# Kernel tuning notes

Measured on AMD Instinct MI355X. Metric: run time of the kernel, lower is better.

Reference implementation:

```python
import jax, jax.numpy as jnp
import numpy as np

S = 32        # window size along the 'time' (intra-patch) axis
C = 32        # channels
P = 4         # patch_size; T = P**3 = 64 = 2*S


def setup_inputs() -> dict:
    key = jax.random.key(0)
    k1, k2, k3 = jax.random.split(key, 3)
    x = jax.random.normal(k1, (2, C, 96, 96, 96), dtype=jnp.float32)
    # nn.Linear(S*C, S*C): weight (out,in), bias (out,)
    W = jax.random.normal(k2, (S * C, S * C), dtype=jnp.float32) / np.float32(np.sqrt(S * C))
    b = jax.random.normal(k3, (S * C,), dtype=jnp.float32) * 0.01
    return {"x": x, "W": W, "b": b}


def reference(x, W, b):
    B, Cc, H, Wd, D = x.shape
    Hp, Wp, Dp = H // P, Wd // P, D // P
    T = P ** 3  # intra-patch token count
    # (B,C,H,W,D) -> (B,C,T,H',W',D') -> (B,H',W',D',T,C)
    xr = x.reshape(B, Cc, T, Hp, Wp, Dp).transpose(0, 3, 4, 5, 2, 1)
    # shift_window: circular roll along T by S//2
    xr = jnp.roll(xr, S // 2, axis=4)
    # group T into windows of S, dense linear over S*C
    xg = xr.reshape(B, Hp, Wp, Dp, T // S, S * Cc)
    y = jnp.einsum('bhwdgk,ok->bhwdgo', xg, W) + b
    # roll back by -(S//2)
    y = jnp.roll(y.reshape(B, Hp, Wp, Dp, T, Cc), -(S // 2), axis=4)
    # (B,H',W',D',T,C) -> (B,C,T,H',W',D') -> (B,C,H,W,D)
    out = y.transpose(0, 5, 4, 1, 2, 3).reshape(B, Cc, H, Wd, D)
    return out
```

## Files before the change

kernel.cpp:

```cpp
#include <hip/hip_runtime.h>


#define NSPAT 884736
#define QQ    13824
#define MTOT  55296
#define KK    1024
#define TS    8192

#define NBLK_A  6912
#define NBLK_W  128

typedef __attribute__((ext_vector_type(4))) float f32x4;
typedef __attribute__((ext_vector_type(8))) short bf16x8;

__device__ __forceinline__ short f2bf(float f) {
  unsigned u = __builtin_bit_cast(unsigned, f);
  u += 0x7fff + ((u >> 16) & 1);
  return (short)(u >> 16);
}

__device__ __forceinline__ void async16(short* lds, const short* g) {
  __builtin_amdgcn_global_load_lds(
      (const __attribute__((address_space(1))) unsigned*)g,
      (__attribute__((address_space(3))) unsigned*)lds, 16, 0, 0);
}

__global__ __launch_bounds__(256)
void convert_pre(const float* __restrict__ x, const float* __restrict__ Wm,
                 short* __restrict__ Abf, short* __restrict__ Wbf) {
  const int bid = blockIdx.x;
  const int tid = threadIdx.x;
  if (bid < NBLK_A) {
    const int mt = bid >> 4;
    const int kt = bid & 15;
    const int seg = mt / 108;
    const int q0  = (mt - seg * 108) * 128;
    const int bb  = seg >> 1;
    const int g   = seg & 1;

    const int rg = tid >> 3;
    const int oc = tid & 7;
    const int jp    = oc >> 2;
    const int cbase = (oc & 3) * 8;
    const int tsrc  = ((g << 5) + kt * 2 + jp + 48) & 63;

    const float* base = x + ((size_t)bb * 32 + cbase) * NSPAT
                          + (size_t)tsrc * QQ + q0 + rg * 4;
    bf16x8 o[4];
#pragma unroll
    for (int tt = 0; tt < 8; tt++) {
      const f32x4 v = *(const f32x4*)(base + (size_t)tt * NSPAT);
#pragma unroll
      for (int r = 0; r < 4; r++) o[r][tt] = f2bf(v[r]);
    }
    short* dst = Abf + (size_t)(mt * 16 + kt) * TS + (rg * 4) * 64 + oc * 8;
#pragma unroll
    for (int r = 0; r < 4; r++)
      *(bf16x8*)(dst + r * 64) = o[r];
  } else {
    const int wb = bid - NBLK_A;
    const int nt = wb >> 4;
    const int kt = wb & 15;
    const int n0 = nt * 128;
#pragma unroll
    for (int it = 0; it < 4; it++) {
      const int idx = it * 256 + tid;
      const int row = idx >> 3;
      const int oc2 = idx & 7;
      const float* wsrc = Wm + (size_t)(n0 + row) * 1024 + kt * 64 + oc2 * 8;
      const f32x4 a = *(const f32x4*)(wsrc);
      const f32x4 b = *(const f32x4*)(wsrc + 4);
      bf16x8 f;
#pragma unroll
      for (int t = 0; t < 4; t++) { f[t] = f2bf(a[t]); f[t + 4] = f2bf(b[t]); }
      *(bf16x8*)(Wbf + (size_t)wb * TS + row * 64 + oc2 * 8) = f;
    }
  }
}

__global__ __launch_bounds__(256, 2)
void swin_mfma(const short* __restrict__ A, const short* __restrict__ Bw,
               const float* __restrict__ bias, float* __restrict__ out) {
  __shared__ __align__(16) short As[128 * 64];
  __shared__ __align__(16) short Bs[128 * 64];

  const int b0 = blockIdx.x;
  const int logical = (b0 & 7) * 432 + (b0 >> 3);
  const int nt = logical & 7;
  const int mt = logical >> 3;
  const int seg = mt / 108;
  const int q0  = (mt - seg * 108) * 128;
  const int bb  = seg >> 1;
  const int g   = seg & 1;
  const int n0  = nt * 128;

  const int tid  = threadIdx.x;
  const int wv   = tid >> 6;
  const int lane = tid & 63;
  const int wr   = wv >> 1;
  const int wc   = wv & 1;
  const int lm   = lane & 15;
  const int quad = lane >> 4;

  const short* aT = A  + (size_t)mt * 16 * TS + wv * 2048 + lane * 8;
  const short* bT = Bw + (size_t)nt * 16 * TS + wv * 2048 + lane * 8;
  short* aL = As + wv * 32 * 64;
  short* bL = Bs + wv * 32 * 64;

  f32x4 acc[4][4];
#pragma unroll
  for (int i = 0; i < 4; i++)
#pragma unroll
    for (int jj = 0; jj < 4; jj++) {
      f32x4 z = {0.f, 0.f, 0.f, 0.f};
      acc[i][jj] = z;
    }

  for (int kt = 0; kt < 16; kt++) {
    const size_t kof = (size_t)kt * TS;
#pragma unroll
    for (int is = 0; is < 4; is++) {
      async16(aL + is * 8 * 64, aT + kof + is * 512);
      async16(bL + is * 8 * 64, bT + kof + is * 512);
    }
    __syncthreads();
#pragma unroll
    for (int ks = 0; ks < 2; ks++) {
      bf16x8 af[4], bfr[4];
#pragma unroll
      for (int i = 0; i < 4; i++)
        af[i] = *(const bf16x8*)(As + (wr * 64 + i * 16 + lm) * 64 + ks * 32 + quad * 8);
#pragma unroll
      for (int jj = 0; jj < 4; jj++)
        bfr[jj] = *(const bf16x8*)(Bs + (wc * 64 + jj * 16 + lm) * 64 + ks * 32 + quad * 8);
#pragma unroll
      for (int i = 0; i < 4; i++)
#pragma unroll
        for (int jj = 0; jj < 4; jj++)
          acc[i][jj] = __builtin_amdgcn_mfma_f32_16x16x32_bf16(af[i], bfr[jj], acc[i][jj], 0, 0, 0);
    }
    __syncthreads();
  }

  float* ob = out + (size_t)bb * 32 * NSPAT;
#pragma unroll
  for (int jj = 0; jj < 4; jj++) {
    const int o  = n0 + wc * 64 + jj * 16 + lm;
    const float bv = bias[o];
    const int so = o >> 5;
    const int cc = o & 31;
    const int tt = ((g << 5) + so + 48) & 63;
    float* orow = ob + (size_t)cc * NSPAT + (size_t)tt * QQ + q0;
#pragma unroll
    for (int i = 0; i < 4; i++) {
      const int mb = wr * 64 + i * 16 + quad * 4;
      f32x4 v = acc[i][jj];
      v += bv;
      *(f32x4*)(orow + mb) = v;
    }
  }
}

__global__ __launch_bounds__(256, 2)
void swin_gemm(const float* __restrict__ x, const float* __restrict__ Wm,
               const float* __restrict__ bias, float* __restrict__ out) {
  const int bid = blockIdx.x;
  const int nt  = bid & 7;
  const int mt  = bid >> 3;
  const int seg = mt / 108;
  const int q0  = (mt - seg * 108) * 128;
  const int bb  = seg >> 1;
  const int g   = seg & 1;

  const int tid  = threadIdx.x;
  const int wv   = tid >> 6;
  const int wr   = wv >> 1;
  const int wc   = wv & 1;
  const int lane = tid & 63;
  const int lm   = lane & 15;
  const int quad = lane >> 4;

  const int n0 = nt * 128 + wc * 64;

  int aoff[4];
#pragma unroll
  for (int i = 0; i < 4; i++)
    aoff[i] = (quad * 8) * NSPAT + q0 + wr * 64 + i * 16 + lm;

  const float* wptr[4];
#pragma unroll
  for (int j = 0; j < 4; j++)
    wptr[j] = Wm + (size_t)(n0 + j * 16 + lm) * 1024 + quad * 8;

  f32x4 acc[4][4];
#pragma unroll
  for (int i = 0; i < 4; i++)
#pragma unroll
    for (int j = 0; j < 4; j++) {
      f32x4 z = {0.f, 0.f, 0.f, 0.f};
      acc[i][j] = z;
    }

  const float* xb = x + (size_t)bb * 32 * NSPAT;

  for (int kc = 0; kc < 32; kc++) {
    const int t_src = ((g << 5) + kc + 48) & 63;
    const float* xs = xb + (size_t)t_src * QQ;

    bf16x8 af[4];
#pragma unroll
    for (int i = 0; i < 4; i++) {
      float v[8];
#pragma unroll
      for (int t = 0; t < 8; t++)
        v[t] = xs[aoff[i] + t * NSPAT];
      bf16x8 f;
#pragma unroll
      for (int t = 0; t < 8; t++) f[t] = f2bf(v[t]);
      af[i] = f;
    }

    bf16x8 bfr[4];
#pragma unroll
    for (int j = 0; j < 4; j++) {
      const float* wp = wptr[j] + kc * 32;
      const f32x4 w0 = *(const f32x4*)(wp);
      const f32x4 w1 = *(const f32x4*)(wp + 4);
      bf16x8 f;
#pragma unroll
      for (int t = 0; t < 4; t++) { f[t] = f2bf(w0[t]); f[t + 4] = f2bf(w1[t]); }
      bfr[j] = f;
    }

#pragma unroll
    for (int i = 0; i < 4; i++)
#pragma unroll
      for (int j = 0; j < 4; j++)
        acc[i][j] = __builtin_amdgcn_mfma_f32_16x16x32_bf16(af[i], bfr[j], acc[i][j], 0, 0, 0);
  }

  float* ob = out + (size_t)bb * 32 * NSPAT;
#pragma unroll
  for (int j = 0; j < 4; j++) {
    const int o  = n0 + j * 16 + lm;
    const float bv = bias[o];
    const int so = o >> 5;
    const int cc = o & 31;
    const int tt = ((g << 5) + so + 48) & 63;
    float* orow = ob + (size_t)cc * NSPAT + (size_t)tt * QQ + q0;
#pragma unroll
    for (int i = 0; i < 4; i++) {
      const int mb = wr * 64 + i * 16 + quad * 4;
      f32x4 v = acc[i][j];
      v += bv;
      *(f32x4*)(orow + mb) = v;
    }
  }
}

extern "C" void kernel_launch(void* const* d_in, const int* in_sizes, int n_in,
                              void* d_out, int out_size, void* d_ws, size_t ws_size,
                              hipStream_t stream) {
  const float* x    = (const float*)d_in[0];
  const float* Wm   = (const float*)d_in[1];
  const float* bias = (const float*)d_in[2];
  float* out        = (float*)d_out;

  const size_t need = (size_t)MTOT * KK * 2 + (size_t)KK * KK * 2;
  if (ws_size >= need) {
    short* Abf = (short*)d_ws;
    short* Wbf = (short*)d_ws + (size_t)MTOT * KK;
    convert_pre<<<dim3(NBLK_A + NBLK_W), dim3(256), 0, stream>>>(x, Wm, Abf, Wbf);
    swin_mfma<<<dim3(432 * 8), dim3(256), 0, stream>>>(Abf, Wbf, bias, out);
  } else {
    swin_gemm<<<dim3(432 * 8), dim3(256), 0, stream>>>(x, Wm, bias, out);
  }
}
```

Measured before the change: 530.4 us.

## Fuse activation fp32-to-bf16 conversion into GEMM and swizzle LDS tiles

Drops the separate pass that converted and re-laid out the activations into a bf16 workspace. The GEMM now loads fp32 x directly, converts it and writes it into LDS, so a full bf16 copy of A is no longer written and re-read through HBM. Both LDS tiles use an XOR swizzle, applied to the weight buffer at conversion time, to reduce bank conflicts. The trade-off is that each of the 8 N-tile blocks re-reads and re-converts the same fp32 activation tile, and these loads are synchronous rather than async-to-LDS.

After: 567.1 us. 1.07x slower.

```diff
diff --git a/kernel.cpp b/kernel.cpp
--- a/kernel.cpp
+++ b/kernel.cpp
@@ -7,9 +7,6 @@
 #define KK    1024
 #define TS    8192
 
-#define NBLK_A  6912
-#define NBLK_W  128
-
 typedef __attribute__((ext_vector_type(4))) float f32x4;
 typedef __attribute__((ext_vector_type(8))) short bf16x8;
 
@@ -26,61 +23,31 @@
 }
 
 __global__ __launch_bounds__(256)
-void convert_pre(const float* __restrict__ x, const float* __restrict__ Wm,
-                 short* __restrict__ Abf, short* __restrict__ Wbf) {
-  const int bid = blockIdx.x;
+void convert_w(const float* __restrict__ Wm, short* __restrict__ Wbf) {
+  const int wb = blockIdx.x;
   const int tid = threadIdx.x;
-  if (bid < NBLK_A) {
-    const int mt = bid >> 4;
-    const int kt = bid & 15;
-    const int seg = mt / 108;
-    const int q0  = (mt - seg * 108) * 128;
-    const int bb  = seg >> 1;
-    const int g   = seg & 1;
-
-    const int rg = tid >> 3;
-    const int oc = tid & 7;
-    const int jp    = oc >> 2;
-    const int cbase = (oc & 3) * 8;
-    const int tsrc  = ((g << 5) + kt * 2 + jp + 48) & 63;
-
-    const float* base = x + ((size_t)bb * 32 + cbase) * NSPAT
-                          + (size_t)tsrc * QQ + q0 + rg * 4;
-    bf16x8 o[4];
-#pragma unroll
-    for (int tt = 0; tt < 8; tt++) {
-      const f32x4 v = *(const f32x4*)(base + (size_t)tt * NSPAT);
-#pragma unroll
-      for (int r = 0; r < 4; r++) o[r][tt] = f2bf(v[r]);
-    }
-    short* dst = Abf + (size_t)(mt * 16 + kt) * TS + (rg * 4) * 64 + oc * 8;
-#pragma unroll
-    for (int r = 0; r < 4; r++)
-      *(bf16x8*)(dst + r * 64) = o[r];
-  } else {
-    const int wb = bid - NBLK_A;
-    const int nt = wb >> 4;
-    const int kt = wb & 15;
-    const int n0 = nt * 128;
-#pragma unroll
-    for (int it = 0; it < 4; it++) {
-      const int idx = it * 256 + tid;
-      const int row = idx >> 3;
-      const int oc2 = idx & 7;
-      const float* wsrc = Wm + (size_t)(n0 + row) * 1024 + kt * 64 + oc2 * 8;
-      const f32x4 a = *(const f32x4*)(wsrc);
-      const f32x4 b = *(const f32x4*)(wsrc + 4);
-      bf16x8 f;
-#pragma unroll
-      for (int t = 0; t < 4; t++) { f[t] = f2bf(a[t]); f[t + 4] = f2bf(b[t]); }
-      *(bf16x8*)(Wbf + (size_t)wb * TS + row * 64 + oc2 * 8) = f;
-    }
+  const int nt = wb >> 4;
+  const int kt = wb & 15;
+  const int n0 = nt * 128;
+#pragma unroll
+  for (int it = 0; it < 4; it++) {
+    const int idx = it * 256 + tid;
+    const int row = idx >> 3;
+    const int oc  = idx & 7;
+    const float* wsrc = Wm + (size_t)(n0 + row) * 1024 + kt * 64 + oc * 8;
+    const f32x4 a = *(const f32x4*)(wsrc);
+    const f32x4 b = *(const f32x4*)(wsrc + 4);
+    bf16x8 f;
+#pragma unroll
+    for (int t = 0; t < 4; t++) { f[t] = f2bf(a[t]); f[t + 4] = f2bf(b[t]); }
+    const int swz = (oc * 8) ^ ((row & 7) << 3);
+    *(bf16x8*)(Wbf + (size_t)wb * TS + row * 64 + swz) = f;
   }
 }
 
 __global__ __launch_bounds__(256, 2)
-void swin_mfma(const short* __restrict__ A, const short* __restrict__ Bw,
-               const float* __restrict__ bias, float* __restrict__ out) {
+void swin_fused(const float* __restrict__ x, const short* __restrict__ Bw,
+                const float* __restrict__ bias, float* __restrict__ out) {
   __shared__ __align__(16) short As[128 * 64];
   __shared__ __align__(16) short Bs[128 * 64];
 
@@ -102,10 +69,22 @@
   const int lm   = lane & 15;
   const int quad = lane >> 4;
 
-  const short* aT = A  + (size_t)mt * 16 * TS + wv * 2048 + lane * 8;
+  const int rg = tid >> 3;
+  const int oc = tid & 7;
+  const int jp = oc >> 2;
+  const int cb = (oc & 3) * 8;
+  const float* xbase = x + ((size_t)bb * 32 + cb) * NSPAT + q0 + rg * 4;
+  int awof[4];
+#pragma unroll
+  for (int r = 0; r < 4; r++) {
+    const int row = rg * 4 + r;
+    awof[r] = row * 64 + ((oc * 8) ^ ((row & 7) << 3));
+  }
+
   const short* bT = Bw + (size_t)nt * 16 * TS + wv * 2048 + lane * 8;
-  short* aL = As + wv * 32 * 64;
-  short* bL = Bs + wv * 32 * 64;
+  short* bL = Bs + wv * 2048;
+
+  const int rsw = (lm & 7) << 3;
 
   f32x4 acc[4][4];
 #pragma unroll
@@ -117,22 +96,36 @@
     }
 
   for (int kt = 0; kt < 16; kt++) {
-    const size_t kof = (size_t)kt * TS;
-#pragma unroll
-    for (int is = 0; is < 4; is++) {
-      async16(aL + is * 8 * 64, aT + kof + is * 512);
-      async16(bL + is * 8 * 64, bT + kof + is * 512);
-    }
+#pragma unroll
+    for (int is = 0; is < 4; is++)
+      async16(bL + is * 512, bT + (size_t)kt * TS + is * 512);
+
+    const int tsrc = ((g << 5) + (kt << 1) + jp + 48) & 63;
+    const float* src = xbase + (size_t)tsrc * QQ;
+    bf16x8 o[4];
+#pragma unroll
+    for (int tt = 0; tt < 8; tt++) {
+      const f32x4 v = *(const f32x4*)(src + (size_t)tt * NSPAT);
+#pragma unroll
+      for (int r = 0; r < 4; r++) o[r][tt] = f2bf(v[r]);
+    }
+#pragma unroll
+    for (int r = 0; r < 4; r++)
+      *(bf16x8*)(As + awof[r]) = o[r];
+
     __syncthreads();
+
 #pragma unroll
     for (int ks = 0; ks < 2; ks++) {
       bf16x8 af[4], bfr[4];
 #pragma unroll
       for (int i = 0; i < 4; i++)
-        af[i] = *(const bf16x8*)(As + (wr * 64 + i * 16 + lm) * 64 + ks * 32 + quad * 8);
+        af[i] = *(const bf16x8*)(As + (wr * 64 + i * 16 + lm) * 64
+                                    + ((ks * 32 + quad * 8) ^ rsw));
 #pragma unroll
       for (int jj = 0; jj < 4; jj++)
-        bfr[jj] = *(const bf16x8*)(Bs + (wc * 64 + jj * 16 + lm) * 64 + ks * 32 + quad * 8);
+        bfr[jj] = *(const bf16x8*)(Bs + (wc * 64 + jj * 16 + lm) * 64
+                                      + ((ks * 32 + quad * 8) ^ rsw));
 #pragma unroll
       for (int i = 0; i < 4; i++)
 #pragma unroll
@@ -266,12 +259,11 @@
   const float* bias = (const float*)d_in[2];
   float* out        = (float*)d_out;
 
-  const size_t need = (size_t)MTOT * KK * 2 + (size_t)KK * KK * 2;
+  const size_t need = (size_t)KK * KK * 2;
   if (ws_size >= need) {
-    short* Abf = (short*)d_ws;
-    short* Wbf = (short*)d_ws + (size_t)MTOT * KK;
-    convert_pre<<<dim3(NBLK_A + NBLK_W), dim3(256), 0, stream>>>(x, Wm, Abf, Wbf);
-    swin_mfma<<<dim3(432 * 8), dim3(256), 0, stream>>>(Abf, Wbf, bias, out);
+    short* Wbf = (short*)d_ws;
+    convert_w<<<dim3(128), dim3(256), 0, stream>>>(Wm, Wbf);
+    swin_fused<<<dim3(432 * 8), dim3(256), 0, stream>>>(x, Wbf, bias, out);
   } else {
     swin_gemm<<<dim3(432 * 8), dim3(256), 0, stream>>>(x, Wm, bias, out);
   }
```
